# Kernel tuning notes

Measured on AMD Instinct MI355X. Metric: run time of the kernel, lower is better.

Reference implementation:

```python
import jax, jax.numpy as jnp
import numpy as np
from jax import lax

B, CIN, COUT, H, W = 8, 128, 128, 128, 128
HID = COUT // 2  # expansion 0.5
K = 3            # kernel size
PAD = 1


def silu(v):
    return v * jax.nn.sigmoid(v)


def base_conv1x1(x, w, s, b):
    # 1x1 conv (no bias) + folded-BN affine (scale s, bias b) + SiLU
    y = jnp.einsum('bchw,oc->bohw', x, w)
    return silu(y * s[None, :, None, None] + b[None, :, None, None])


def bilinear_gather(img, py, px):
    Hin, Win = img.shape[1], img.shape[2]
    y0 = jnp.floor(py)
    x0 = jnp.floor(px)
    wy = py - y0
    wx = px - x0

    def corner(yc, xc):
        valid = (yc >= 0) & (yc <= Hin - 1) & (xc >= 0) & (xc <= Win - 1)
        yi = jnp.clip(yc, 0, Hin - 1).astype(jnp.int32)
        xi = jnp.clip(xc, 0, Win - 1).astype(jnp.int32)
        v = img[:, yi, xi]  # [C, Kk, H, W]
        return v * valid[None].astype(img.dtype)

    v00 = corner(y0, x0)
    v01 = corner(y0, x0 + 1)
    v10 = corner(y0 + 1, x0)
    v11 = corner(y0 + 1, x0 + 1)
    wy = wy[None]
    wx = wx[None]
    return (v00 * (1 - wy) * (1 - wx) + v01 * (1 - wy) * wx
            + v10 * wy * (1 - wx) + v11 * wy * wx)


def deform_conv_depthwise(x, off_w, off_b, dw):
    # x: [B, C, H, W]; off_w: [2*K*K, C, 3, 3]; dw: [C, K, K] (depthwise, groups=C)
    b, c, h, w = x.shape
    off = lax.conv_general_dilated(
        x, off_w, window_strides=(1, 1), padding=((PAD, PAD), (PAD, PAD)),
        dimension_numbers=('NCHW', 'OIHW', 'NCHW'))
    off = off + off_b[None, :, None, None]
    off = off.reshape(b, K * K, 2, h, w)  # torchvision: (dy, dx) per tap
    dy, dx = off[:, :, 0], off[:, :, 1]   # [B, 9, H, W]

    ky = jnp.repeat(jnp.arange(K, dtype=x.dtype), K)  # [9]
    kx = jnp.tile(jnp.arange(K, dtype=x.dtype), K)
    yy = jnp.arange(h, dtype=x.dtype)[None, :, None]  # [1, H, 1]
    xx = jnp.arange(w, dtype=x.dtype)[None, None, :]
    py = yy + ky[:, None, None] - PAD  # [9, H, W]
    px = xx + kx[:, None, None] - PAD
    py = py[None] + dy  # [B, 9, H, W]
    px = px[None] + dx

    sampled = jax.vmap(bilinear_gather)(x, py, px)  # [B, C, 9, H, W]
    return jnp.einsum('bckhw,ck->bchw', sampled, dw.reshape(c, K * K))


def setup_inputs() -> dict:
    key = jax.random.key(0)
    ks = jax.random.split(key, 12)
    f = jnp.float32
    inp = {
        'x': jax.random.normal(ks[0], (B, CIN, H, W), f),
        'w1': jax.random.normal(ks[1], (HID, CIN), f) * 0.05,
        's1': jnp.ones((HID,), f), 'b1': jnp.zeros((HID,), f),
        'w2': jax.random.normal(ks[2], (HID, CIN), f) * 0.05,
        's2': jnp.ones((HID,), f), 'b2': jnp.zeros((HID,), f),
        'w3': jax.random.normal(ks[3], (COUT, 2 * HID), f) * 0.05,
        's3': jnp.ones((COUT,), f), 'b3': jnp.zeros((COUT,), f),
        'off_w': jax.random.normal(ks[4], (2 * K * K, HID, K, K), f) * 0.01,
        'off_b': jnp.zeros((2 * K * K,), f),
        'dw': jax.random.normal(ks[5], (HID, K, K), f) * 0.1,
    }
    return inp


def reference(x, w1, s1, b1, w2, s2, b2, w3, s3, b3, off_w, off_b, dw):
    x1 = base_conv1x1(x, w1, s1, b1)          # [B, HID, H, W]
    x2 = base_conv1x1(x, w2, s2, b2)          # [B, HID, H, W]
    x1 = deform_conv_depthwise(x1, off_w, off_b, dw)
    xc = jnp.concatenate([x1, x2], axis=1)    # [B, 2*HID, H, W]
    return base_conv1x1(xc, w3, s3, b3)       # [B, COUT, H, W]
```

## Files before the change

kernel.cpp:

```cpp
#include <hip/hip_runtime.h>

typedef unsigned short u16;
typedef unsigned int   u32;
typedef unsigned char  u8;

#define BB    8
#define CINC  128
#define HIDC  64
#define COUTC 128
#define HH    128
#define WWD   128
#define HWN   16384
#define NPOS  (BB*HWN)

typedef __attribute__((ext_vector_type(8))) short bf16x8;
typedef __attribute__((ext_vector_type(4))) float f32x4;

__device__ __forceinline__ float b2f(u16 u){
    union { u32 i; float f; } v; v.i = ((u32)u) << 16; return v.f;
}
__device__ __forceinline__ u16 f2b(float f){
    union { float f; u32 i; } v; v.f = f;
    u32 i = v.i;
    i += 0x7fffu + ((i >> 16) & 1u);
    return (u16)(i >> 16);
}
__device__ __forceinline__ float blo(u32 u){
    union { u32 i; float f; } v; v.i = u << 16; return v.f;
}
__device__ __forceinline__ float bhi(u32 u){
    union { u32 i; float f; } v; v.i = u & 0xFFFF0000u; return v.f;
}
__device__ __forceinline__ float silu(float y){
    return y / (1.f + __expf(-y));
}

template<bool ISB>
__device__ __forceinline__ float ldp(const void* p, int i){
    if (ISB) return b2f(((const u16*)p)[i]);
    return ((const float*)p)[i];
}

template<bool ISB>
__device__ __forceinline__ void k0_body(
    const void* w1, const void* s1, const void* b1,
    const void* w2, const void* s2, const void* b2,
    const void* w3, const void* s3, const void* b3,
    const void* offw, const void* offb, const void* dw,
    u16* __restrict__ wbc, u16* __restrict__ wb3,
    float* __restrict__ bfc, float* __restrict__ bf3,
    u16* __restrict__ wA, float* __restrict__ ob32, float* __restrict__ dwfT)
{
    int t = blockIdx.x*256 + threadIdx.x;
    if (t < 8192){
        wbc[t] = f2b(ldp<ISB>(w1,t) * ldp<ISB>(s1,t>>7));
    } else if (t < 16384){
        int u = t - 8192;
        wbc[t] = f2b(ldp<ISB>(w2,u) * ldp<ISB>(s2,u>>7));
    }
    if (t < 16384){
        wb3[t] = f2b(ldp<ISB>(w3,t) * ldp<ISB>(s3,t>>7));
    }
    if (t < 18432){
        int set  = t / 9216, rem = t % 9216;
        int tap  = rem / 1024; int rem2 = rem % 1024;
        int chunk= rem2 >> 9;  int rem3 = rem2 & 511;
        int lane = rem3 >> 3;  int jp   = rem3 & 7;
        int jg   = set*16 + (lane & 15);
        int c    = chunk*32 + (lane>>4)*8 + jp;
        float v  = (jg < 18) ? ldp<ISB>(offw, (jg*HIDC + c)*9 + tap) : 0.f;
        wA[t] = f2b(v);
    }
    if (t < HIDC)  bfc[t]      = ldp<ISB>(b1,t);
    if (t >= HIDC && t < 2*HIDC) bfc[t] = ldp<ISB>(b2,t-HIDC);
    if (t < COUTC) bf3[t] = ldp<ISB>(b3,t);
    if (t < 32)    ob32[t] = (t < 18) ? ldp<ISB>(offb,t) : 0.f;
    if (t < HIDC*9){
        int c = t / 9, k = t % 9;
        dwfT[k*HIDC + c] = ldp<ISB>(dw,t);
    }
}

__global__ __launch_bounds__(256) void k0_prep(
    const void* w1, const void* s1, const void* b1,
    const void* w2, const void* s2, const void* b2,
    const void* w3, const void* s3, const void* b3,
    const void* offw, const void* offb, const void* dw,
    u16* wbc, u16* wb3, float* bfc, float* bf3,
    u16* wA, float* ob32, float* dwfT)
{
    bool isb = (((const u32*)s1)[0] == 0x3F803F80u);
    if (isb) k0_body<true >(w1,s1,b1,w2,s2,b2,w3,s3,b3,offw,offb,dw,wbc,wb3,bfc,bf3,wA,ob32,dwfT);
    else     k0_body<false>(w1,s1,b1,w2,s2,b2,w3,s3,b3,offw,offb,dw,wbc,wb3,bfc,bf3,wA,ob32,dwfT);
}

template<bool ISB>
__device__ __forceinline__ void k1_body(const void* __restrict__ xv,
    const u16* __restrict__ wbc, const float* __restrict__ bfc,
    u16* __restrict__ x1, u16* __restrict__ x2, u8* __restrict__ sx8)
{
    const int posb = blockIdx.x*64;
    const int bidx = posb >> 14;
    const int hwb  = posb & (HWN-1);

    {
        const int R  = threadIdx.x >> 2;
        const int qq = threadIdx.x & 3;
        u32* dst = (u32*)(sx8 + R*272 + qq*64);
        if (ISB){
            const u16* r0 = (const u16*)xv + (size_t)bidx*CINC*HWN + (size_t)(2*R)*HWN + hwb + qq*16;
            const u16* r1 = r0 + HWN;
            uint4 a0 = *(const uint4*)(r0);
            uint4 a1 = *(const uint4*)(r0 + 8);
            uint4 c0 = *(const uint4*)(r1);
            uint4 c1 = *(const uint4*)(r1 + 8);
            u32 A[8] = {a0.x,a0.y,a0.z,a0.w,a1.x,a1.y,a1.z,a1.w};
            u32 C[8] = {c0.x,c0.y,c0.z,c0.w,c1.x,c1.y,c1.z,c1.w};
            #pragma unroll
            for (int k = 0; k < 8; ++k){
                dst[2*k]   = (A[k] & 0xFFFFu) | (C[k] << 16);
                dst[2*k+1] = (A[k] >> 16)     | (C[k] & 0xFFFF0000u);
            }
        } else {
            const float* r0 = (const float*)xv + (size_t)bidx*CINC*HWN + (size_t)(2*R)*HWN + hwb + qq*16;
            const float* r1 = r0 + HWN;
            #pragma unroll
            for (int k = 0; k < 8; ++k){
                float2 f0 = *(const float2*)(r0 + 2*k);
                float2 f1 = *(const float2*)(r1 + 2*k);
                dst[2*k]   = (u32)f2b(f0.x) | ((u32)f2b(f1.x) << 16);
                dst[2*k+1] = (u32)f2b(f0.y) | ((u32)f2b(f1.y) << 16);
            }
        }
    }
    __syncthreads();

    const int w    = threadIdx.x >> 6;
    const int lane = threadIdx.x & 63;
    const int n    = lane & 15;
    const int quad = lane >> 4;

    bf16x8 wf[2][4];
    #pragma unroll
    for (int m = 0; m < 2; ++m)
        #pragma unroll
        for (int t = 0; t < 4; ++t)
            wf[m][t] = *(const bf16x8*)(wbc + (size_t)(w*32 + m*16 + n)*CINC + t*32 + quad*8);

    f32x4 acc[2][4];
    #pragma unroll
    for (int m = 0; m < 2; ++m)
        #pragma unroll
        for (int s = 0; s < 4; ++s) acc[m][s] = (f32x4){0.f,0.f,0.f,0.f};

    #pragma unroll
    for (int t = 0; t < 4; ++t){
        #pragma unroll
        for (int sub = 0; sub < 4; ++sub){
            union { u32 u[4]; bf16x8 v; } bb;
            #pragma unroll
            for (int jp = 0; jp < 4; ++jp)
                bb.u[jp] = *(const u32*)(sx8 + (t*16 + quad*4 + jp)*272 + (sub*16 + n)*4);
            acc[0][sub] = __builtin_amdgcn_mfma_f32_16x16x32_bf16(wf[0][t], bb.v, acc[0][sub], 0,0,0);
            acc[1][sub] = __builtin_amdgcn_mfma_f32_16x16x32_bf16(wf[1][t], bb.v, acc[1][sub], 0,0,0);
        }
    }

    #pragma unroll
    for (int m = 0; m < 2; ++m){
        const int ob = w*32 + m*16 + quad*4;
        float4 bi = *(const float4*)(bfc + ob);
        u16* dbuf = (ob < 64) ? x1 : x2;
        const int oo = ob & 63;
        #pragma unroll
        for (int sub = 0; sub < 4; ++sub){
            const u32 lo = (u32)f2b(silu(acc[m][sub][0] + bi.x))
                         | ((u32)f2b(silu(acc[m][sub][1] + bi.y)) << 16);
            const u32 hi = (u32)f2b(silu(acc[m][sub][2] + bi.z))
                         | ((u32)f2b(silu(acc[m][sub][3] + bi.w)) << 16);
            *(uint2*)(dbuf + (size_t)(posb + sub*16 + n)*HIDC + oo) = make_uint2(lo, hi);
        }
    }
}

__global__ __launch_bounds__(256) void k1_mfma(const void* x, const u32* s1probe,
    const u16* wbc, const float* bfc, u16* x1, u16* x2)
{
    __shared__ __align__(16) u8 sx8[64*272];
    bool isb = (s1probe[0] == 0x3F803F80u);
    if (isb) k1_body<true >(x, wbc, bfc, x1, x2, sx8);
    else     k1_body<false>(x, wbc, bfc, x1, x2, sx8);
}

__global__ __launch_bounds__(256) void k2_mfma(const u16* __restrict__ x1,
    const u16* __restrict__ wA, const float* __restrict__ ob32,
    float* __restrict__ offT)
{
    const int lane = threadIdx.x & 63;
    const int n    = lane & 15;
    const int quad = lane >> 4;
    const int tile = blockIdx.x*4 + (threadIdx.x >> 6);
    const int posbase = tile*16;
    const int b   = posbase >> 14;
    const int hw  = posbase & (HWN-1);
    const int y   = hw >> 7;
    const int x0  = hw & (WWD-1);
    const int xb  = x0 + n - 1;
    const u16* bbase = x1 + (size_t)b*HWN*HIDC;

    f32x4 acc0 = (f32x4){0.f,0.f,0.f,0.f};
    f32x4 acc1 = (f32x4){0.f,0.f,0.f,0.f};

    #pragma unroll
    for (int ky = 0; ky < 3; ++ky){
        int ys = y + ky - 1;
        if ((unsigned)ys >= HH) continue;
        const u16* rowp = bbase + (size_t)ys*WWD*HIDC;
        #pragma unroll
        for (int kx = 0; kx < 3; ++kx){
            int  xs  = xb + kx;
            int  xcl = min(max(xs, 0), WWD-1);
            bool vx  = ((unsigned)xs < WWD);
            const int tap = ky*3 + kx;
            #pragma unroll
            for (int ch = 0; ch < 2; ++ch){
                bf16x8 bfr = *(const bf16x8*)(rowp + xcl*HIDC + ch*32 + quad*8);
                if (!vx) bfr = (bf16x8){0,0,0,0,0,0,0,0};
                bf16x8 a0 = *(const bf16x8*)(wA + ((0*9 + tap)*2 + ch)*512 + lane*8);
                bf16x8 a1 = *(const bf16x8*)(wA + ((1*9 + tap)*2 + ch)*512 + lane*8);
                acc0 = __builtin_amdgcn_mfma_f32_16x16x32_bf16(a0, bfr, acc0, 0,0,0);
                acc1 = __builtin_amdgcn_mfma_f32_16x16x32_bf16(a1, bfr, acc1, 0,0,0);
            }
        }
    }
    #pragma unroll
    for (int r = 0; r < 4; ++r){
        int j0 = quad*4 + r;
        offT[(size_t)j0*NPOS + posbase + n] = acc0[r] + ob32[j0];
        int j1 = 16 + quad*4 + r;
        if (j1 < 18)
            offT[(size_t)j1*NPOS + posbase + n] = acc1[r] + ob32[j1];
    }
}

__global__ __launch_bounds__(256, 2) void k3b_gather(const u16* __restrict__ x1,
    const float* __restrict__ offT, const float* __restrict__ dwfT,
    u16* __restrict__ x1d)
{
    __shared__ float s_dwf[576];
    __shared__ __align__(16) u8 s_meta[16*208];

    const int tid  = threadIdx.x;
    if (tid < 144)
        *(float4*)(s_dwf + tid*4) = *(const float4*)(dwfT + tid*4);

    const int lane = tid & 63;
    const int gw   = blockIdx.x*4 + (tid >> 6);
    const int posw = gw << 2;
    const int p    = lane >> 4;
    const int li   = lane & 15;
    const int pos  = posw + p;
    const int slot = (tid >> 4) * 208;

    if (li < 9){
        const int k = li;
        int hw = pos & (HWN-1);
        int y  = hw >> 7, x = hw & (WWD-1);
        float dy = offT[(size_t)(2*k  )*NPOS + pos];
        float dx = offT[(size_t)(2*k+1)*NPOS + pos];
        float py = (float)(y + k/3 - 1) + dy;
        float px = (float)(x + k%3 - 1) + dx;
        float fy = floorf(py), fx = floorf(px);
        float wy = py - fy,    wx = px - fx;
        int y0 = (int)fy, x0i = (int)fx;
        float vy0 = ((unsigned)y0      < HH)  ? 1.f : 0.f;
        float vy1 = ((unsigned)(y0+1)  < HH)  ? 1.f : 0.f;
        float vx0 = ((unsigned)x0i     < WWD) ? 1.f : 0.f;
        float vx1 = ((unsigned)(x0i+1) < WWD) ? 1.f : 0.f;
        int yc0 = min(max(y0,   0), HH-1),  yc1 = min(max(y0+1, 0), HH-1);
        int xc0 = min(max(x0i,  0), WWD-1), xc1 = min(max(x0i+1, 0), WWD-1);
        float wy1 = 1.f - wy, wx1 = 1.f - wx;
        float4 w4;
        w4.x = wy1*wx1*vy0*vx0;
        w4.y = wy1*wx *vy0*vx1;
        w4.z = wy *wx1*vy1*vx0;
        w4.w = wy *wx *vy1*vx1;
        int o0 = (yc0*WWD + xc0)*HIDC;
        int sx = (xc1 != xc0) ? 1 : 0;
        int sy = (yc1 != yc0) ? 1 : 0;
        *(int*)   (s_meta + slot + 4*k)       = o0 | (sx<<20) | (sy<<21);
        *(float4*)(s_meta + slot + 48 + 16*k) = w4;
    }
    __syncthreads();

    const int b = posw >> 14;
    const u32* xb32 = (const u32*)(x1 + (size_t)b*HWN*HIDC) + li*2;

    float acc0 = 0.f, acc1 = 0.f, acc2 = 0.f, acc3 = 0.f;
    #pragma unroll
    for (int k = 0; k < 9; ++k){
        const int    pk  = *(const int*)   (s_meta + slot + 4*k);
        const float4 f   = *(const float4*)(s_meta + slot + 48 + 16*k);
        const float4 dwf = *(const float4*)(s_dwf + k*HIDC + li*4);
        const int o0  = (pk & 0xFFFFF) >> 1;
        const int dxs = (pk & (1<<20)) ? (HIDC>>1)       : 0;
        const int dys = (pk & (1<<21)) ? ((WWD*HIDC)>>1) : 0;
        const uint2 q00 = *(const uint2*)(xb32 + o0);
        const uint2 q01 = *(const uint2*)(xb32 + o0 + dxs);
        const uint2 q10 = *(const uint2*)(xb32 + o0 + dys);
        const uint2 q11 = *(const uint2*)(xb32 + o0 + dys + dxs);

        float s0 = blo(q00.x)*f.x + blo(q01.x)*f.y + blo(q10.x)*f.z + blo(q11.x)*f.w;
        float s1 = bhi(q00.x)*f.x + bhi(q01.x)*f.y + bhi(q10.x)*f.z + bhi(q11.x)*f.w;
        float s2 = blo(q00.y)*f.x + blo(q01.y)*f.y + blo(q10.y)*f.z + blo(q11.y)*f.w;
        float s3 = bhi(q00.y)*f.x + bhi(q01.y)*f.y + bhi(q10.y)*f.z + bhi(q11.y)*f.w;
        acc0 += s0*dwf.x;
        acc1 += s1*dwf.y;
        acc2 += s2*dwf.z;
        acc3 += s3*dwf.w;
    }

    const u32 r0 = ((u32)f2b(acc1) << 16) | (u32)f2b(acc0);
    const u32 r1 = ((u32)f2b(acc3) << 16) | (u32)f2b(acc2);
    uint2* outp = (uint2*)((u32*)x1d + (size_t)pos*(HIDC/2) + li*2);
    *outp = make_uint2(r0, r1);
}

template<bool ISB>
__device__ __forceinline__ void k4_body(const u16* __restrict__ x1d,
    const u16* __restrict__ x2,
    const u16* __restrict__ wb3, const float* __restrict__ bf3,
    void* __restrict__ out)
{
    const int posb = blockIdx.x*64;
    const int bidx = posb >> 14;
    const int hwb  = posb & (HWN-1);
    const int w    = threadIdx.x >> 6;
    const int lane = threadIdx.x & 63;
    const int n    = lane & 15;
    const int quad = lane >> 4;

    bf16x8 wf[2][4];
    #pragma unroll
    for (int m = 0; m < 2; ++m)
        #pragma unroll
        for (int t = 0; t < 4; ++t)
            wf[m][t] = *(const bf16x8*)(wb3 + (size_t)(w*32 + m*16 + n)*CINC + t*32 + quad*8);

    f32x4 acc[2][4];
    #pragma unroll
    for (int m = 0; m < 2; ++m)
        #pragma unroll
        for (int s = 0; s < 4; ++s) acc[m][s] = (f32x4){0.f,0.f,0.f,0.f};

    #pragma unroll
    for (int t = 0; t < 4; ++t){
        const u16* src = (t < 2) ? x1d : x2;
        #pragma unroll
        for (int sub = 0; sub < 4; ++sub){
            bf16x8 bfr = *(const bf16x8*)(src + (size_t)(posb + sub*16 + n)*HIDC + (t&1)*32 + quad*8);
            acc[0][sub] = __builtin_amdgcn_mfma_f32_16x16x32_bf16(wf[0][t], bfr, acc[0][sub], 0,0,0);
            acc[1][sub] = __builtin_amdgcn_mfma_f32_16x16x32_bf16(wf[1][t], bfr, acc[1][sub], 0,0,0);
        }
    }

    u16*   ob16 = (u16*)  out + (size_t)bidx*COUTC*HWN + hwb;
    float* obf  = (float*)out + (size_t)bidx*COUTC*HWN + hwb;
    #pragma unroll
    for (int m = 0; m < 2; ++m){
        const int ob = w*32 + m*16 + quad*4;
        float4 bi = *(const float4*)(bf3 + ob);
        #pragma unroll
        for (int sub = 0; sub < 4; ++sub){
            const int pp = sub*16 + n;
            #pragma unroll
            for (int r = 0; r < 4; ++r){
                const float bv = (r==0)?bi.x:(r==1)?bi.y:(r==2)?bi.z:bi.w;
                const float v = silu(acc[m][sub][r] + bv);
                if (ISB) ob16[(size_t)(ob+r)*HWN + pp] = f2b(v);
                else     obf [(size_t)(ob+r)*HWN + pp] = v;
            }
        }
    }
}

__global__ __launch_bounds__(256) void k4_mfma(const u16* x1d, const u16* x2,
    const u32* s1probe, const u16* wb3, const float* bf3, void* out)
{
    bool isb = (s1probe[0] == 0x3F803F80u);
    if (isb) k4_body<true >(x1d, x2, wb3, bf3, out);
    else     k4_body<false>(x1d, x2, wb3, bf3, out);
}

extern "C" void kernel_launch(void* const* d_in, const int* in_sizes, int n_in,
                              void* d_out, int out_size, void* d_ws, size_t ws_size,
                              hipStream_t stream)
{
    const void* x    = d_in[0];
    const void* w1   = d_in[1];
    const void* s1   = d_in[2];
    const void* b1   = d_in[3];
    const void* w2   = d_in[4];
    const void* s2   = d_in[5];
    const void* b2   = d_in[6];
    const void* w3   = d_in[7];
    const void* s3   = d_in[8];
    const void* b3   = d_in[9];
    const void* offw = d_in[10];
    const void* offb = d_in[11];
    const void* dw   = d_in[12];

    char* ws = (char*)d_ws;
    u16*   x1    = (u16*)  (ws + 0);
    u16*   x2    = (u16*)  (ws + 16777216);
    u16*   x1d   = (u16*)  (ws + 33554432);
    float* offT  = (float*)(ws + 50331648);
    u16*   wbc   = (u16*)  (ws + 59768832);
    u16*   wb3   = (u16*)  (ws + 59801600);
    u16*   wA    = (u16*)  (ws + 59834368);
    float* dwfT  = (float*)(ws + 59871232);
    float* bfc   = (float*)(ws + 59873536);
    float* bf3   = (float*)(ws + 59874048);
    float* ob32  = (float*)(ws + 59874560);

    k0_prep<<<72, 256, 0, stream>>>(w1,s1,b1, w2,s2,b2, w3,s3,b3, offw,offb,dw,
                                    wbc, wb3, bfc, bf3, wA, ob32, dwfT);
    k1_mfma  <<<NPOS/64, 256, 0, stream>>>(x, (const u32*)s1, wbc, bfc, x1, x2);
    k2_mfma  <<<2048, 256, 0, stream>>>(x1, wA, ob32, offT);
    k3b_gather<<<NPOS/16, 256, 0, stream>>>(x1, offT, dwfT, x1d);
    k4_mfma  <<<NPOS/64, 256, 0, stream>>>(x1d, x2, (const u32*)s1, wb3, bf3, d_out);
}
```

Measured before the change: 242.2 us.

## Fuse offset conv and deformable gather into one kernel via shared memory

Merges the MFMA offset-convolution kernel with the bilinear gather kernel, so the 18 offset channels per position stay in shared memory instead of going through a global offT buffer. This removes one launch plus the offset write and re-read. The gather stage is also reworked so each lane loads 8 channels with 16-byte loads, covering 8 positions per iteration. In exchange the block does both phases with extra barriers, uses more shared memory, and has fewer blocks to overlap memory latency.

```diff
diff --git a/kernel.cpp b/kernel.cpp
--- a/kernel.cpp
+++ b/kernel.cpp
@@ -192,82 +192,79 @@
     else     k1_body<false>(x, wbc, bfc, x1, x2, sx8);
 }
 
-__global__ __launch_bounds__(256) void k2_mfma(const u16* __restrict__ x1,
+__global__ __launch_bounds__(256, 2) void k23_fused(const u16* __restrict__ x1,
     const u16* __restrict__ wA, const float* __restrict__ ob32,
-    float* __restrict__ offT)
-{
-    const int lane = threadIdx.x & 63;
-    const int n    = lane & 15;
-    const int quad = lane >> 4;
-    const int tile = blockIdx.x*4 + (threadIdx.x >> 6);
-    const int posbase = tile*16;
-    const int b   = posbase >> 14;
-    const int hw  = posbase & (HWN-1);
-    const int y   = hw >> 7;
-    const int x0  = hw & (WWD-1);
-    const int xb  = x0 + n - 1;
-    const u16* bbase = x1 + (size_t)b*HWN*HIDC;
-
-    f32x4 acc0 = (f32x4){0.f,0.f,0.f,0.f};
-    f32x4 acc1 = (f32x4){0.f,0.f,0.f,0.f};
-
-    #pragma unroll
-    for (int ky = 0; ky < 3; ++ky){
-        int ys = y + ky - 1;
-        if ((unsigned)ys >= HH) continue;
-        const u16* rowp = bbase + (size_t)ys*WWD*HIDC;
-        #pragma unroll
-        for (int kx = 0; kx < 3; ++kx){
-            int  xs  = xb + kx;
-            int  xcl = min(max(xs, 0), WWD-1);
-            bool vx  = ((unsigned)xs < WWD);
-            const int tap = ky*3 + kx;
-            #pragma unroll
-            for (int ch = 0; ch < 2; ++ch){
-                bf16x8 bfr = *(const bf16x8*)(rowp + xcl*HIDC + ch*32 + quad*8);
-                if (!vx) bfr = (bf16x8){0,0,0,0,0,0,0,0};
-                bf16x8 a0 = *(const bf16x8*)(wA + ((0*9 + tap)*2 + ch)*512 + lane*8);
-                bf16x8 a1 = *(const bf16x8*)(wA + ((1*9 + tap)*2 + ch)*512 + lane*8);
-                acc0 = __builtin_amdgcn_mfma_f32_16x16x32_bf16(a0, bfr, acc0, 0,0,0);
-                acc1 = __builtin_amdgcn_mfma_f32_16x16x32_bf16(a1, bfr, acc1, 0,0,0);
-            }
-        }
-    }
-    #pragma unroll
-    for (int r = 0; r < 4; ++r){
-        int j0 = quad*4 + r;
-        offT[(size_t)j0*NPOS + posbase + n] = acc0[r] + ob32[j0];
-        int j1 = 16 + quad*4 + r;
-        if (j1 < 18)
-            offT[(size_t)j1*NPOS + posbase + n] = acc1[r] + ob32[j1];
-    }
-}
-
-__global__ __launch_bounds__(256, 2) void k3b_gather(const u16* __restrict__ x1,
-    const float* __restrict__ offT, const float* __restrict__ dwfT,
-    u16* __restrict__ x1d)
+    const float* __restrict__ dwfT, u16* __restrict__ x1d)
 {
     __shared__ float s_dwf[576];
-    __shared__ __align__(16) u8 s_meta[16*208];
+    __shared__ float s_offs[64*21];
+    __shared__ int   s_offi[64*12];
+    __shared__ __align__(16) float4 s_facs[64*9];
 
     const int tid  = threadIdx.x;
     if (tid < 144)
         *(float4*)(s_dwf + tid*4) = *(const float4*)(dwfT + tid*4);
 
+    const int w    = tid >> 6;
     const int lane = tid & 63;
-    const int gw   = blockIdx.x*4 + (tid >> 6);
-    const int posw = gw << 2;
-    const int p    = lane >> 4;
-    const int li   = lane & 15;
-    const int pos  = posw + p;
-    const int slot = (tid >> 4) * 208;
-
-    if (li < 9){
-        const int k = li;
+    const int n    = lane & 15;
+    const int quad = lane >> 4;
+    const int posb = blockIdx.x*64;
+    const int b    = posb >> 14;
+    const u16* bbase = x1 + (size_t)b*HWN*HIDC;
+
+    {
+        const int posbase = posb + w*16;
+        const int hw  = posbase & (HWN-1);
+        const int y   = hw >> 7;
+        const int x0  = hw & (WWD-1);
+        const int xb  = x0 + n - 1;
+
+        f32x4 acc0 = (f32x4){0.f,0.f,0.f,0.f};
+        f32x4 acc1 = (f32x4){0.f,0.f,0.f,0.f};
+
+        #pragma unroll
+        for (int ky = 0; ky < 3; ++ky){
+            int ys = y + ky - 1;
+            if ((unsigned)ys >= HH) continue;
+            const u16* rowp = bbase + (size_t)ys*WWD*HIDC;
+            #pragma unroll
+            for (int kx = 0; kx < 3; ++kx){
+                int  xs  = xb + kx;
+                int  xcl = min(max(xs, 0), WWD-1);
+                bool vx  = ((unsigned)xs < WWD);
+                const int tap = ky*3 + kx;
+                #pragma unroll
+                for (int ch = 0; ch < 2; ++ch){
+                    bf16x8 bfr = *(const bf16x8*)(rowp + xcl*HIDC + ch*32 + quad*8);
+                    if (!vx) bfr = (bf16x8){0,0,0,0,0,0,0,0};
+                    bf16x8 a0 = *(const bf16x8*)(wA + ((0*9 + tap)*2 + ch)*512 + lane*8);
+                    bf16x8 a1 = *(const bf16x8*)(wA + ((1*9 + tap)*2 + ch)*512 + lane*8);
+                    acc0 = __builtin_amdgcn_mfma_f32_16x16x32_bf16(a0, bfr, acc0, 0,0,0);
+                    acc1 = __builtin_amdgcn_mfma_f32_16x16x32_bf16(a1, bfr, acc1, 0,0,0);
+                }
+            }
+        }
+        const int pl = w*16 + n;
+        #pragma unroll
+        for (int r = 0; r < 4; ++r){
+            int j0 = quad*4 + r;
+            s_offs[pl*21 + j0] = acc0[r] + ob32[j0];
+            int j1 = 16 + quad*4 + r;
+            if (j1 < 18)
+                s_offs[pl*21 + j1] = acc1[r] + ob32[j1];
+        }
+    }
+    __syncthreads();
+
+    for (int task = tid; task < 576; task += 256){
+        int pl = task / 9;
+        int k  = task - pl*9;
+        int pos = posb + pl;
         int hw = pos & (HWN-1);
         int y  = hw >> 7, x = hw & (WWD-1);
-        float dy = offT[(size_t)(2*k  )*NPOS + pos];
-        float dx = offT[(size_t)(2*k+1)*NPOS + pos];
+        float dy = s_offs[pl*21 + 2*k];
+        float dx = s_offs[pl*21 + 2*k + 1];
         float py = (float)(y + k/3 - 1) + dy;
         float px = (float)(x + k%3 - 1) + dx;
         float fy = floorf(py), fx = floorf(px);
@@ -288,42 +285,50 @@
         int o0 = (yc0*WWD + xc0)*HIDC;
         int sx = (xc1 != xc0) ? 1 : 0;
         int sy = (yc1 != yc0) ? 1 : 0;
-        *(int*)   (s_meta + slot + 4*k)       = o0 | (sx<<20) | (sy<<21);
-        *(float4*)(s_meta + slot + 48 + 16*k) = w4;
+        s_offi[pl*12 + k] = o0 | (sx<<20) | (sy<<21);
+        s_facs[pl*9 + k]  = w4;
     }
     __syncthreads();
 
-    const int b = posw >> 14;
-    const u32* xb32 = (const u32*)(x1 + (size_t)b*HWN*HIDC) + li*2;
-
-    float acc0 = 0.f, acc1 = 0.f, acc2 = 0.f, acc3 = 0.f;
-    #pragma unroll
-    for (int k = 0; k < 9; ++k){
-        const int    pk  = *(const int*)   (s_meta + slot + 4*k);
-        const float4 f   = *(const float4*)(s_meta + slot + 48 + 16*k);
-        const float4 dwf = *(const float4*)(s_dwf + k*HIDC + li*4);
-        const int o0  = (pk & 0xFFFFF) >> 1;
-        const int dxs = (pk & (1<<20)) ? (HIDC>>1)       : 0;
-        const int dys = (pk & (1<<21)) ? ((WWD*HIDC)>>1) : 0;
-        const uint2 q00 = *(const uint2*)(xb32 + o0);
-        const uint2 q01 = *(const uint2*)(xb32 + o0 + dxs);
-        const uint2 q10 = *(const uint2*)(xb32 + o0 + dys);
-        const uint2 q11 = *(const uint2*)(xb32 + o0 + dys + dxs);
-
-        float s0 = blo(q00.x)*f.x + blo(q01.x)*f.y + blo(q10.x)*f.z + blo(q11.x)*f.w;
-        float s1 = bhi(q00.x)*f.x + bhi(q01.x)*f.y + bhi(q10.x)*f.z + bhi(q11.x)*f.w;
-        float s2 = blo(q00.y)*f.x + blo(q01.y)*f.y + blo(q10.y)*f.z + blo(q11.y)*f.w;
-        float s3 = bhi(q00.y)*f.x + bhi(q01.y)*f.y + bhi(q10.y)*f.z + bhi(q11.y)*f.w;
-        acc0 += s0*dwf.x;
-        acc1 += s1*dwf.y;
-        acc2 += s2*dwf.z;
-        acc3 += s3*dwf.w;
-    }
-
-    const u32 r0 = ((u32)f2b(acc1) << 16) | (u32)f2b(acc0);
-    const u32 r1 = ((u32)f2b(acc3) << 16) | (u32)f2b(acc2);
-    uint2* outp = (uint2*)((u32*)x1d + (size_t)pos*(HIDC/2) + li*2);
-    *outp = make_uint2(r0, r1);
+    const int cg = lane & 7;
+    const u32* xb32 = (const u32*)bbase + cg*4;
+    #pragma unroll
+    for (int it = 0; it < 2; ++it){
+        const int posl = w*16 + it*8 + (lane >> 3);
+        const int pos  = posb + posl;
+        float acc[8];
+        #pragma unroll
+        for (int j = 0; j < 8; ++j) acc[j] = 0.f;
+        #pragma unroll
+        for (int k = 0; k < 9; ++k){
+            const int    pk = s_offi[posl*12 + k];
+            const float4 f  = s_facs[posl*9 + k];
+            const float4 d0 = *(const float4*)(s_dwf + k*HIDC + cg*8);
+            const float4 d1 = *(const float4*)(s_dwf + k*HIDC + cg*8 + 4);
+            const int o0  = (pk & 0xFFFFF) >> 1;
+            const int dxs = (pk & (1<<20)) ? (HIDC>>1)       : 0;
+            const int dys = (pk & (1<<21)) ? ((WWD*HIDC)>>1) : 0;
+            const uint4 q00 = *(const uint4*)(xb32 + o0);
+            const uint4 q01 = *(const uint4*)(xb32 + o0 + dxs);
+            const uint4 q10 = *(const uint4*)(xb32 + o0 + dys);
+            const uint4 q11 = *(const uint4*)(xb32 + o0 + dys + dxs);
+            #define BIL(J, C00, C01, C10, C11, DLO, DHI) { \
+                float slo = blo(C00)*f.x + blo(C01)*f.y + blo(C10)*f.z + blo(C11)*f.w; \
+                float shi = bhi(C00)*f.x + bhi(C01)*f.y + bhi(C10)*f.z + bhi(C11)*f.w; \
+                acc[2*(J)]   += slo*(DLO); \
+                acc[2*(J)+1] += shi*(DHI); }
+            BIL(0, q00.x, q01.x, q10.x, q11.x, d0.x, d0.y)
+            BIL(1, q00.y, q01.y, q10.y, q11.y, d0.z, d0.w)
+            BIL(2, q00.z, q01.z, q10.z, q11.z, d1.x, d1.y)
+            BIL(3, q00.w, q01.w, q10.w, q11.w, d1.z, d1.w)
+            #undef BIL
+        }
+        const u32 r0 = (u32)f2b(acc[0]) | ((u32)f2b(acc[1]) << 16);
+        const u32 r1 = (u32)f2b(acc[2]) | ((u32)f2b(acc[3]) << 16);
+        const u32 r2 = (u32)f2b(acc[4]) | ((u32)f2b(acc[5]) << 16);
+        const u32 r3 = (u32)f2b(acc[6]) | ((u32)f2b(acc[7]) << 16);
+        *(uint4*)(x1d + (size_t)pos*HIDC + cg*8) = make_uint4(r0, r1, r2, r3);
+    }
 }
 
 template<bool ISB>
@@ -414,7 +419,6 @@
     u16*   x1    = (u16*)  (ws + 0);
     u16*   x2    = (u16*)  (ws + 16777216);
     u16*   x1d   = (u16*)  (ws + 33554432);
-    float* offT  = (float*)(ws + 50331648);
     u16*   wbc   = (u16*)  (ws + 59768832);
     u16*   wb3   = (u16*)  (ws + 59801600);
     u16*   wA    = (u16*)  (ws + 59834368);
@@ -426,7 +430,6 @@
     k0_prep<<<72, 256, 0, stream>>>(w1,s1,b1, w2,s2,b2, w3,s3,b3, offw,offb,dw,
                                     wbc, wb3, bfc, bf3, wA, ob32, dwfT);
     k1_mfma  <<<NPOS/64, 256, 0, stream>>>(x, (const u32*)s1, wbc, bfc, x1, x2);
-    k2_mfma  <<<2048, 256, 0, stream>>>(x1, wA, ob32, offT);
-    k3b_gather<<<NPOS/16, 256, 0, stream>>>(x1, offT, dwfT, x1d);
+    k23_fused<<<NPOS/64, 256, 0, stream>>>(x1, wA, ob32, dwfT, x1d);
     k4_mfma  <<<NPOS/64, 256, 0, stream>>>(x1d, x2, (const u32*)s1, wb3, bf3, d_out);
 }
```

Measured after the change: 228.4 us. 5.7% less time.
